# Kernel tuning notes

Hardware: AMD Instinct MI355X
Metric: run time of the kernel (lower is better)

## Reference

```python
import jax, jax.numpy as jnp
import numpy as np

B, T, E, H = 8, 2048, 1024, 64

def setup_inputs() -> dict:
    key = jax.random.key(0)
    k1, k2, k3, k4 = jax.random.split(key, 4)
    x = jax.random.normal(k1, (B, T, E), dtype=jnp.float32)
    # match nn.Linear init scale roughly (values only affect numerics, not math)
    s = 1.0 / np.sqrt(E)
    Wk = jax.random.normal(k2, (E, H), dtype=jnp.float32) * s
    Wq = jax.random.normal(k3, (E, H), dtype=jnp.float32) * s
    Wv = jax.random.normal(k4, (E, H), dtype=jnp.float32) * s
    return {"x": x, "Wk": Wk, "Wq": Wq, "Wv": Wv}

def reference(x, Wk, Wq, Wv):
    # projections: [B,T,E] @ [E,H] -> [B,T,H]
    k = x @ Wk
    q = x @ Wq
    v = x @ Wv
    scale = k.shape[-1] ** -0.5
    # scores [B,T,T]
    scores = jnp.einsum('bth,bsh->bts', q, k) * scale
    Tq = x.shape[1]
    causal = jnp.tril(jnp.ones((Tq, Tq), dtype=bool))
    scores = jnp.where(causal, scores, -jnp.inf)
    weights = jax.nn.softmax(scores, axis=-1)
    # dropout p=0.0 -> identity
    att = jnp.einsum('bts,bsh->bth', weights, v)  # [B,T,H]
    return att
```

## Files before the change

kernel.cpp:

```cpp
#include <hip/hip_runtime.h>
#include <hip/hip_bf16.h>

typedef _Float16 f16;
typedef _Float16 f16x8 __attribute__((ext_vector_type(8)));
typedef float f32x4 __attribute__((ext_vector_type(4)));

#define NB 8
#define NT 2048
#define NE 1024
#define NH 64

#define CHUNKS_PER_BATCH 144
#define MAXC 8

#define OFF_WT 0
#define OFF_QH 393216
#define OFF_KH 2490368
#define OFF_VT 4587520
#define OFF_ML 6684672
#define OFF_OP 7733248

__global__ __launch_bounds__(256) void wconv_kernel(
        const float* __restrict__ Wk, const float* __restrict__ Wq,
        const float* __restrict__ Wv, f16* __restrict__ wt) {
    __shared__ float tile[64][65];
    const int mat = blockIdx.x >> 4;
    const int e0 = (blockIdx.x & 15) * 64;
    const float* W = (mat == 0) ? Wq : (mat == 1) ? Wk : Wv;
    const int tx = threadIdx.x & 63;
    const int ty = threadIdx.x >> 6;
#pragma unroll
    for (int r = ty; r < 64; r += 4)
        tile[r][tx] = W[(size_t)(e0 + r) * NH + tx];
    __syncthreads();
#pragma unroll
    for (int h = ty; h < 64; h += 4)
        wt[(size_t)mat * (NH * NE) + (size_t)h * NE + e0 + tx] = (f16)tile[tx][h];
}

__global__ __launch_bounds__(256) void qkv_proj_kernel(
        const float* __restrict__ x, const f16* __restrict__ wt,
        f16* __restrict__ Qh, f16* __restrict__ Kh, f16* __restrict__ VT) {
    __shared__ f16 xs[2][64 * 64];
    __shared__ f16 wsb[2][192 * 64];

    const int tid = threadIdx.x;
    const int wave = tid >> 6;
    const int lane = tid & 63;
    const int lr = lane & 15;
    const int lg = lane >> 4;
    const int m0 = blockIdx.x * 64;
    const int nt0 = wave * 3;

    f32x4 acc[12] = {};

    float4 xr0, xr1, xr2, xr3;
    int4 wr0, wr1, wr2, wr3, wr4, wr5;

    const int xrow = tid >> 2;
    const int xcg = (tid & 3) * 16;

#define ISSUE_LOADS(kc)                                                        \
    do {                                                                       \
        const float* xb = x + (size_t)(m0 + xrow) * NE + (kc) + xcg;           \
        xr0 = *(const float4*)(xb);                                            \
        xr1 = *(const float4*)(xb + 4);                                        \
        xr2 = *(const float4*)(xb + 8);                                        \
        xr3 = *(const float4*)(xb + 12);                                       \
        wr0 = *(const int4*)(wt + (size_t)((tid + 0 * 256) >> 3) * NE + (kc) + ((tid + 0 * 256) & 7) * 8); \
        wr1 = *(const int4*)(wt + (size_t)((tid + 1 * 256) >> 3) * NE + (kc) + ((tid + 1 * 256) & 7) * 8); \
        wr2 = *(const int4*)(wt + (size_t)((tid + 2 * 256) >> 3) * NE + (kc) + ((tid + 2 * 256) & 7) * 8); \
        wr3 = *(const int4*)(wt + (size_t)((tid + 3 * 256) >> 3) * NE + (kc) + ((tid + 3 * 256) & 7) * 8); \
        wr4 = *(const int4*)(wt + (size_t)((tid + 4 * 256) >> 3) * NE + (kc) + ((tid + 4 * 256) & 7) * 8); \
        wr5 = *(const int4*)(wt + (size_t)((tid + 5 * 256) >> 3) * NE + (kc) + ((tid + 5 * 256) & 7) * 8); \
    } while (0)

#define CVT8(dst, a0, a1)                                                      \
    f16x8 dst = { (f16)a0.x, (f16)a0.y, (f16)a0.z, (f16)a0.w,                  \
                  (f16)a1.x, (f16)a1.y, (f16)a1.z, (f16)a1.w }

#define WRITE_LDS(buf)                                                         \
    do {                                                                       \
        { CVT8(v0, xr0, xr1);                                                  \
          int c = (tid & 3) * 2;                                               \
          int byo = xrow * 128 + ((c * 16) ^ ((xrow & 7) << 4));               \
          *(f16x8*)((char*)xs[buf] + byo) = v0; }                              \
        { CVT8(v1, xr2, xr3);                                                  \
          int c = (tid & 3) * 2 + 1;                                           \
          int byo = xrow * 128 + ((c * 16) ^ ((xrow & 7) << 4));               \
          *(f16x8*)((char*)xs[buf] + byo) = v1; }                              \
        { int jw = tid + 0 * 256, n = jw >> 3, c = jw & 7;                     \
          *(int4*)((char*)wsb[buf] + n * 128 + ((c * 16) ^ ((n & 7) << 4))) = wr0; } \
        { int jw = tid + 1 * 256, n = jw >> 3, c = jw & 7;                     \
          *(int4*)((char*)wsb[buf] + n * 128 + ((c * 16) ^ ((n & 7) << 4))) = wr1; } \
        { int jw = tid + 2 * 256, n = jw >> 3, c = jw & 7;                     \
          *(int4*)((char*)wsb[buf] + n * 128 + ((c * 16) ^ ((n & 7) << 4))) = wr2; } \
        { int jw = tid + 3 * 256, n = jw >> 3, c = jw & 7;                     \
          *(int4*)((char*)wsb[buf] + n * 128 + ((c * 16) ^ ((n & 7) << 4))) = wr3; } \
        { int jw = tid + 4 * 256, n = jw >> 3, c = jw & 7;                     \
          *(int4*)((char*)wsb[buf] + n * 128 + ((c * 16) ^ ((n & 7) << 4))) = wr4; } \
        { int jw = tid + 5 * 256, n = jw >> 3, c = jw & 7;                     \
          *(int4*)((char*)wsb[buf] + n * 128 + ((c * 16) ^ ((n & 7) << 4))) = wr5; } \
    } while (0)

    ISSUE_LOADS(0);
    WRITE_LDS(0);
    __syncthreads();

    int cur = 0;
    for (int c = 0; c < 16; ++c) {
        if (c < 15) ISSUE_LOADS((c + 1) * 64);

#pragma unroll
        for (int ks = 0; ks < 2; ++ks) {
            f16x8 af[4], bf[3];
#pragma unroll
            for (int mt = 0; mt < 4; ++mt) {
                int row = mt * 16 + lr;
                int byo = row * 128 + ((ks * 64 + lg * 16) ^ ((row & 7) << 4));
                af[mt] = *(const f16x8*)((const char*)xs[cur] + byo);
            }
#pragma unroll
            for (int j = 0; j < 3; ++j) {
                int n = (nt0 + j) * 16 + lr;
                int byo = n * 128 + ((ks * 64 + lg * 16) ^ ((n & 7) << 4));
                bf[j] = *(const f16x8*)((const char*)wsb[cur] + byo);
            }
#pragma unroll
            for (int mt = 0; mt < 4; ++mt)
#pragma unroll
                for (int j = 0; j < 3; ++j)
                    acc[mt * 3 + j] = __builtin_amdgcn_mfma_f32_16x16x32_f16(
                        af[mt], bf[j], acc[mt * 3 + j], 0, 0, 0);
        }

        __syncthreads();
        if (c < 15) {
            WRITE_LDS(cur ^ 1);
            __syncthreads();
        }
        cur ^= 1;
    }

#pragma unroll
    for (int j = 0; j < 3; ++j) {
        int nbase = (nt0 + j) * 16;
        int mat = nbase >> 6;
        int ncol = (nbase & 63) + lr;
#pragma unroll
        for (int mt = 0; mt < 4; ++mt) {
#pragma unroll
            for (int r = 0; r < 4; ++r) {
                int m = m0 + mt * 16 + lg * 4 + r;
                f16 val = (f16)acc[mt * 3 + j][r];
                if (mat == 0) {
                    Qh[(size_t)m * NH + ncol] = val;
                } else if (mat == 1) {
                    Kh[(size_t)m * NH + ncol] = val;
                } else {
                    int bb = m >> 11;
                    int tt = m & 2047;
                    VT[((size_t)bb * NH + ncol) * NT + tt] = val;
                }
            }
        }
    }
#undef ISSUE_LOADS
#undef CVT8
#undef WRITE_LDS
}

__global__ __launch_bounds__(256) void attn_part_kernel(
        const f16* __restrict__ Qh, const f16* __restrict__ Kh,
        const f16* __restrict__ VT, f16* __restrict__ op, float2* __restrict__ ml) {
    __shared__ f16 pbuf[4][16][72];

    const int wave = threadIdx.x >> 6;
    const int lane = threadIdx.x & 63;
    const int lr = lane & 15;
    const int lg = lane >> 4;

    const int b = blockIdx.x / CHUNKS_PER_BATCH;
    int c = blockIdx.x % CHUNKS_PER_BATCH;
    int qi = 0;
    for (; qi < 32; ++qi) {
        int ncq = (qi + 4) >> 2;
        if (c < ncq) break;
        c -= ncq;
    }
    const int total_steps = (qi + 1) * 2;
    const int sbeg = c * 8;
    const int send = min(sbeg + 8, total_steps);
    const int qbase = qi * 64;
    const int qrow = qbase + wave * 16;

    const f16* Qb = Qh + (size_t)b * NT * NH;
    const f16* Kb = Kh + (size_t)b * NT * NH;
    const f16* Vb = VT + (size_t)b * NH * NT;

    f16x8 qf[2];
#pragma unroll
    for (int h = 0; h < 2; ++h) {
        qf[h] = *(const f16x8*)(Qb + (size_t)(qrow + lr) * NH + h * 32 + lg * 8);
#pragma unroll
        for (int j = 0; j < 8; ++j) qf[h][j] = qf[h][j] * (f16)0.125f;
    }

    f32x4 o[4] = {};
    float mrow[4], lrow[4];
#pragma unroll
    for (int r = 0; r < 4; ++r) { mrow[r] = -INFINITY; lrow[r] = 0.f; }

    for (int s2 = sbeg; s2 < send; s2 += 2) {
        const int s0 = s2 * 32;

        f32x4 S[4] = {};
#pragma unroll
        for (int t = 0; t < 4; ++t) {
#pragma unroll
            for (int h = 0; h < 2; ++h) {
                f16x8 kf = *(const f16x8*)(Kb + (size_t)(s0 + t * 16 + lr) * NH + h * 32 + lg * 8);
                S[t] = __builtin_amdgcn_mfma_f32_16x16x32_f16(qf[h], kf, S[t], 0, 0, 0);
            }
        }

        if (s0 + 63 > qrow) {
#pragma unroll
            for (int t = 0; t < 4; ++t) {
#pragma unroll
                for (int r = 0; r < 4; ++r) {
                    int q = qrow + lg * 4 + r;
                    int key = s0 + t * 16 + lr;
                    S[t][r] = (key <= q) ? S[t][r] : -INFINITY;
                }
            }
        }

        float mx[4];
#pragma unroll
        for (int r = 0; r < 4; ++r)
            mx[r] = fmaxf(fmaxf(S[0][r], S[1][r]), fmaxf(S[2][r], S[3][r]));
#pragma unroll
        for (int d = 1; d < 16; d <<= 1) {
#pragma unroll
            for (int r = 0; r < 4; ++r) mx[r] = fmaxf(mx[r], __shfl_xor(mx[r], d));
        }

        float nms[4];
        bool grow = false;
#pragma unroll
        for (int r = 0; r < 4; ++r) grow = grow || (mx[r] > mrow[r]);
        if (__ballot(grow) != 0ull) {
#pragma unroll
            for (int r = 0; r < 4; ++r) {
                float nm = fmaxf(mrow[r], mx[r]);
                nms[r] = (nm == -INFINITY) ? 0.f : nm;
                float fr = __expf(mrow[r] - nms[r]);
                mrow[r] = nm;
                lrow[r] *= fr;
#pragma unroll
                for (int ht = 0; ht < 4; ++ht) o[ht][r] *= fr;
            }
        } else {
#pragma unroll
            for (int r = 0; r < 4; ++r) nms[r] = (mrow[r] == -INFINITY) ? 0.f : mrow[r];
        }

#pragma unroll
        for (int t = 0; t < 4; ++t) {
#pragma unroll
            for (int r = 0; r < 4; ++r) S[t][r] = __expf(S[t][r] - nms[r]);
        }
#pragma unroll
        for (int r = 0; r < 4; ++r) {
            float rsum = (S[0][r] + S[1][r]) + (S[2][r] + S[3][r]);
#pragma unroll
            for (int d = 1; d < 16; d <<= 1) rsum += __shfl_xor(rsum, d);
            lrow[r] += rsum;
        }

#pragma unroll
        for (int t = 0; t < 4; ++t) {
#pragma unroll
            for (int r = 0; r < 4; ++r)
                pbuf[wave][lg * 4 + r][t * 16 + lr] = (f16)S[t][r];
        }
        __builtin_amdgcn_wave_barrier();
        f16x8 pf0 = *(const f16x8*)(&pbuf[wave][lr][lg * 8]);
        f16x8 pf1 = *(const f16x8*)(&pbuf[wave][lr][32 + lg * 8]);

#pragma unroll
        for (int ht = 0; ht < 4; ++ht) {
            f16x8 vf0 = *(const f16x8*)(Vb + (size_t)(ht * 16 + lr) * NT + s0 + lg * 8);
            f16x8 vf1 = *(const f16x8*)(Vb + (size_t)(ht * 16 + lr) * NT + s0 + 32 + lg * 8);
            o[ht] = __builtin_amdgcn_mfma_f32_16x16x32_f16(pf0, vf0, o[ht], 0, 0, 0);
            o[ht] = __builtin_amdgcn_mfma_f32_16x16x32_f16(pf1, vf1, o[ht], 0, 0, 0);
        }
        __builtin_amdgcn_wave_barrier();
    }

#pragma unroll
    for (int r = 0; r < 4; ++r) {
        int qt = qrow + lg * 4 + r;
        size_t slot = ((size_t)b * NT + qt) * MAXC + c;
#pragma unroll
        for (int ht = 0; ht < 4; ++ht)
            op[slot * NH + ht * 16 + lr] = (f16)o[ht][r];
        if (lr == 0) {
            float2 v; v.x = mrow[r]; v.y = lrow[r];
            ml[slot] = v;
        }
    }
}

__global__ __launch_bounds__(256) void combine_kernel(
        const f16* __restrict__ op, const float2* __restrict__ ml,
        float* __restrict__ out) {
    int gid = blockIdx.x * 256 + threadIdx.x;
    int row = gid >> 6;
    int h = gid & 63;
    int q = row & (NT - 1);
    int qi = q >> 6;
    int nc = (qi + 4) >> 2;

    size_t base = (size_t)row * MAXC;
    float2 ml0 = ml[base];
    float M = ml0.x, L = ml0.y;
    float O = (float)op[base * NH + h];
    for (int cc = 1; cc < nc; ++cc) {
        float2 mlc = ml[base + cc];
        if (mlc.x == -INFINITY) continue;
        float oc = (float)op[(base + cc) * NH + h];
        float nM = fmaxf(M, mlc.x);
        float wo = __expf(M - nM), wc = __expf(mlc.x - nM);
        O = O * wo + oc * wc;
        L = L * wo + mlc.y * wc;
        M = nM;
    }
    out[gid] = O / L;
}

extern "C" void kernel_launch(void* const* d_in, const int* in_sizes, int n_in,
                              void* d_out, int out_size, void* d_ws, size_t ws_size,
                              hipStream_t stream) {
    const float* x  = (const float*)d_in[0];
    const float* Wk = (const float*)d_in[1];
    const float* Wq = (const float*)d_in[2];
    const float* Wv = (const float*)d_in[3];
    float* out = (float*)d_out;

    char* ws = (char*)d_ws;
    f16* wt    = (f16*)(ws + OFF_WT);
    f16* Qh    = (f16*)(ws + OFF_QH);
    f16* Kh    = (f16*)(ws + OFF_KH);
    f16* VT    = (f16*)(ws + OFF_VT);
    float2* ml = (float2*)(ws + OFF_ML);
    f16* op    = (f16*)(ws + OFF_OP);

    hipLaunchKernelGGL(wconv_kernel, dim3(48), dim3(256), 0, stream, Wk, Wq, Wv, wt);
    hipLaunchKernelGGL(qkv_proj_kernel, dim3(256), dim3(256), 0, stream, x, wt, Qh, Kh, VT);
    hipLaunchKernelGGL(attn_part_kernel, dim3(NB * CHUNKS_PER_BATCH), dim3(256), 0, stream,
                       Qh, Kh, VT, op, ml);
    hipLaunchKernelGGL(combine_kernel, dim3(NB * NT * NH / 256), dim3(256), 0, stream,
                       op, ml, out);
}
```

Measured before the change: 175.5 us.

## Stage K/V tiles through double-buffered swizzled LDS shared across waves

Each block now loads the 64x64 K and V tiles once into LDS with an XOR swizzle, instead of every wave reading them directly from global memory. The next tile is prefetched into registers while the current tile is computed, then written to the other LDS buffer. This cuts redundant global/L2 traffic (previously four waves each fetched the same K/V) and overlaps loads with MFMA work. The cost is a block-wide __syncthreads per step and 32KB of extra LDS, which may lower occupancy.

```diff
diff --git a/kernel.cpp b/kernel.cpp
--- a/kernel.cpp
+++ b/kernel.cpp
@@ -173,10 +173,13 @@
 __global__ __launch_bounds__(256) void attn_part_kernel(
         const f16* __restrict__ Qh, const f16* __restrict__ Kh,
         const f16* __restrict__ VT, f16* __restrict__ op, float2* __restrict__ ml) {
+    __shared__ f16 kbuf[2][64 * 64];
+    __shared__ f16 vbuf[2][64 * 64];
     __shared__ f16 pbuf[4][16][72];
 
-    const int wave = threadIdx.x >> 6;
-    const int lane = threadIdx.x & 63;
+    const int tid = threadIdx.x;
+    const int wave = tid >> 6;
+    const int lane = tid & 63;
     const int lr = lane & 15;
     const int lg = lane >> 4;
 
@@ -191,6 +194,7 @@
     const int total_steps = (qi + 1) * 2;
     const int sbeg = c * 8;
     const int send = min(sbeg + 8, total_steps);
+    const int nsteps = (send - sbeg) >> 1;
     const int qbase = qi * 64;
     const int qrow = qbase + wave * 16;
 
@@ -198,6 +202,32 @@
     const f16* Kb = Kh + (size_t)b * NT * NH;
     const f16* Vb = VT + (size_t)b * NH * NT;
 
+    const int srow = tid >> 2;
+    const int scol = (tid & 3) * 16;
+    const int scb0 = (tid & 3) * 32;
+    int4 kr0, kr1, vr0, vr1;
+
+#define LOADKV(s0_)                                                            \
+    do {                                                                       \
+        const f16* kp = Kb + (size_t)((s0_) + srow) * NH + scol;               \
+        kr0 = *(const int4*)(kp);                                              \
+        kr1 = *(const int4*)(kp + 8);                                          \
+        const f16* vp = Vb + (size_t)srow * NT + (s0_) + scol;                 \
+        vr0 = *(const int4*)(vp);                                              \
+        vr1 = *(const int4*)(vp + 8);                                          \
+    } while (0)
+
+#define WRITEKV(buf_)                                                          \
+    do {                                                                       \
+        int swz = (srow & 7) << 4;                                             \
+        char* kb = (char*)kbuf[buf_] + srow * 128;                             \
+        *(int4*)(kb + (scb0 ^ swz)) = kr0;                                     \
+        *(int4*)(kb + ((scb0 + 16) ^ swz)) = kr1;                              \
+        char* vb = (char*)vbuf[buf_] + srow * 128;                             \
+        *(int4*)(vb + (scb0 ^ swz)) = vr0;                                     \
+        *(int4*)(vb + ((scb0 + 16) ^ swz)) = vr1;                              \
+    } while (0)
+
     f16x8 qf[2];
 #pragma unroll
     for (int h = 0; h < 2; ++h) {
@@ -211,15 +241,24 @@
 #pragma unroll
     for (int r = 0; r < 4; ++r) { mrow[r] = -INFINITY; lrow[r] = 0.f; }
 
-    for (int s2 = sbeg; s2 < send; s2 += 2) {
-        const int s0 = s2 * 32;
+    LOADKV(sbeg * 32);
+    WRITEKV(0);
+
+    int cur = 0;
+    for (int n = 0; n < nsteps; ++n) {
+        __syncthreads();
+        const int s0 = (sbeg + 2 * n) * 32;
+        if (n + 1 < nsteps) LOADKV((sbeg + 2 * (n + 1)) * 32);
 
         f32x4 S[4] = {};
 #pragma unroll
         for (int t = 0; t < 4; ++t) {
+            int row = t * 16 + lr;
+            const char* kb = (const char*)kbuf[cur] + row * 128;
+            int swz = (row & 7) << 4;
 #pragma unroll
             for (int h = 0; h < 2; ++h) {
-                f16x8 kf = *(const f16x8*)(Kb + (size_t)(s0 + t * 16 + lr) * NH + h * 32 + lg * 8);
+                f16x8 kf = *(const f16x8*)(kb + ((h * 64 + lg * 16) ^ swz));
                 S[t] = __builtin_amdgcn_mfma_f32_16x16x32_f16(qf[h], kf, S[t], 0, 0, 0);
             }
         }
@@ -291,13 +330,21 @@
 
 #pragma unroll
         for (int ht = 0; ht < 4; ++ht) {
-            f16x8 vf0 = *(const f16x8*)(Vb + (size_t)(ht * 16 + lr) * NT + s0 + lg * 8);
-            f16x8 vf1 = *(const f16x8*)(Vb + (size_t)(ht * 16 + lr) * NT + s0 + 32 + lg * 8);
+            int row = ht * 16 + lr;
+            const char* vb = (const char*)vbuf[cur] + row * 128;
+            int swz = (row & 7) << 4;
+            f16x8 vf0 = *(const f16x8*)(vb + ((lg * 16) ^ swz));
+            f16x8 vf1 = *(const f16x8*)(vb + ((64 + lg * 16) ^ swz));
             o[ht] = __builtin_amdgcn_mfma_f32_16x16x32_f16(pf0, vf0, o[ht], 0, 0, 0);
             o[ht] = __builtin_amdgcn_mfma_f32_16x16x32_f16(pf1, vf1, o[ht], 0, 0, 0);
         }
         __builtin_amdgcn_wave_barrier();
-    }
+
+        if (n + 1 < nsteps) WRITEKV(cur ^ 1);
+        cur ^= 1;
+    }
+#undef LOADKV
+#undef WRITEKV
 
 #pragma unroll
     for (int r = 0; r < 4; ++r) {
```

After: 150.2 us. 14.4% less time.
